# Kernel optimization log

Measured on AMD Instinct MI355X. Metric: run time of the kernel, lower is better.

The kernel has to match this reference:

```python
import jax, jax.numpy as jnp
import numpy as np

B, L, H = 32, 512, 1024
Q = 128
VA_H = 256

def setup_inputs() -> dict:
    key = jax.random.key(0)
    ks = jax.random.split(key, 12)
    hidden_states = jax.random.normal(ks[0], (B, L, H), dtype=jnp.float32)
    # Build valid inclusive spans: start in [2, L-16), length in [0, 8)
    asp_s = jax.random.randint(ks[1], (B, Q), 2, L - 16)
    asp_e = asp_s + jax.random.randint(ks[2], (B, Q), 0, 8)
    opi_s = jax.random.randint(ks[3], (B, Q), 2, L - 16)
    opi_e = opi_s + jax.random.randint(ks[4], (B, Q), 0, 8)
    null = jax.random.uniform(ks[5], (B, Q)) < 0.1
    asp_s = jnp.where(null, 0, asp_s)
    quad_spans = jnp.stack([asp_s, asp_e, opi_s, opi_e], axis=-1).astype(jnp.int64)
    quad_mask = (jax.random.uniform(ks[6], (B, Q)) > 0.3).astype(jnp.float32)
    # MLP params (torch Linear: y = x @ W.T + b), kaiming-ish scale
    def lin(k, out_d, in_d):
        return jax.random.normal(k, (out_d, in_d), dtype=jnp.float32) / np.sqrt(in_d)
    W1 = lin(ks[7], VA_H, 3 * H); b1 = jnp.zeros((VA_H,), jnp.float32)
    W2 = lin(ks[8], VA_H // 2, VA_H); b2 = jnp.zeros((VA_H // 2,), jnp.float32)
    W3 = lin(ks[9], 2, VA_H // 2); b3 = jnp.zeros((2,), jnp.float32)
    return {"hidden_states": hidden_states, "quad_spans": quad_spans,
            "quad_mask": quad_mask, "W1": W1, "b1": b1, "W2": W2, "b2": b2,
            "W3": W3, "b3": b3}

def _pool_spans(hidden_states, s, e):
    # hidden_states: [B,L,H]; s,e: [B,Q] inclusive indices
    pos = jnp.arange(hidden_states.shape[1])  # [L]
    valid = (s >= 2) & (e >= s)               # [B,Q]
    m = (pos[None, None, :] >= s[..., None]) & (pos[None, None, :] <= e[..., None])
    m = (m & valid[..., None]).astype(hidden_states.dtype)  # [B,Q,L]
    cnt = jnp.maximum(m.sum(-1, keepdims=True), 1.0)        # [B,Q,1]
    mean = jnp.einsum('bql,blh->bqh', m, hidden_states) / cnt
    sep = hidden_states[:, 1:2, :]                           # [B,1,H] fallback
    return jnp.where(valid[..., None], mean, sep)

def reference(hidden_states, quad_spans, quad_mask, W1, b1, W2, b2, W3, b3):
    h_asp = _pool_spans(hidden_states, quad_spans[..., 0], quad_spans[..., 1])
    h_opi = _pool_spans(hidden_states, quad_spans[..., 2], quad_spans[..., 3])
    h_pair = jnp.concatenate([h_asp, h_opi, h_asp * h_opi], axis=-1)  # [B,Q,3H]
    x = jax.nn.gelu(h_pair @ W1.T + b1, approximate=False)  # torch GELU = erf
    x = jax.nn.gelu(x @ W2.T + b2, approximate=False)
    va = jax.nn.sigmoid(x @ W3.T + b3) * 8.0 + 1.0          # [B,Q,2] in [1,9]
    # Invalid pairs stay zero, matching the torch loop's skipped entries
    return va * (quad_mask >= 0.5).astype(va.dtype)[..., None]
```

## Files before the change

kernel.cpp:

```cpp
#include <hip/hip_runtime.h>
#include <hip/hip_bf16.h>
#include <math.h>

typedef __bf16 bf16x8 __attribute__((ext_vector_type(8)));
typedef float f32x4 __attribute__((ext_vector_type(4)));

__device__ __forceinline__ unsigned short f2bf(float x) {
    union { float f; unsigned int u; } v; v.f = x;
    unsigned int r = v.u + 0x7fffu + ((v.u >> 16) & 1u);
    return (unsigned short)(r >> 16);
}
__device__ __forceinline__ float gelu_exact(float v) {
    return 0.5f * v * (1.0f + erff(v * 0.70710678118654752f));
}

__global__ __launch_bounds__(256) void prep_kernel(const float* __restrict__ hs,
                                                   const int* __restrict__ spans,
                                                   const float* __restrict__ W1,
                                                   const float* __restrict__ W2,
                                                   unsigned short* __restrict__ hp,
                                                   unsigned short* __restrict__ w1b,
                                                   unsigned short* __restrict__ w2b) {
    const int blk = blockIdx.x;
    const int tid = threadIdx.x;

    if (blk >= 4096) {
        if (blk < 4864) {
            const int i = (blk - 4096) * 256 + tid;
            float4 f = ((const float4*)W1)[i];
            ushort4 u;
            u.x = f2bf(f.x); u.y = f2bf(f.y); u.z = f2bf(f.z); u.w = f2bf(f.w);
            ((ushort4*)w1b)[i] = u;
        } else {
            const int i = (blk - 4864) * 256 + tid;
            float4 f = ((const float4*)W2)[i];
            ushort4 u;
            u.x = f2bf(f.x); u.y = f2bf(f.y); u.z = f2bf(f.z); u.w = f2bf(f.w);
            ((ushort4*)w2b)[i] = u;
        }
        return;
    }

    const int pair = blk;
    const int b = pair >> 7;

    const bool is64 = (spans[1] == 0);
    int s_a, e_a, s_o, e_o;
    if (is64) {
        s_a = spans[(pair * 4 + 0) * 2]; e_a = spans[(pair * 4 + 1) * 2];
        s_o = spans[(pair * 4 + 2) * 2]; e_o = spans[(pair * 4 + 3) * 2];
    } else {
        s_a = spans[pair * 4 + 0]; e_a = spans[pair * 4 + 1];
        s_o = spans[pair * 4 + 2]; e_o = spans[pair * 4 + 3];
    }

    if (!(s_a >= 2 && e_a >= s_a)) { s_a = 1; e_a = 1; }
    if (!(s_o >= 2 && e_o >= s_o)) { s_o = 1; e_o = 1; }
    const int lenA = e_a - s_a + 1;
    const int lenO = e_o - s_o + 1;

    const float4* base = (const float4*)hs + (size_t)b * 512 * 256;

    float4 va[8], vo[8];
#pragma unroll
    for (int t = 0; t < 8; ++t) {
        int ra = s_a + t; ra = (ra > e_a) ? e_a : ra;
        int ro = s_o + t; ro = (ro > e_o) ? e_o : ro;
        va[t] = base[ra * 256 + tid];
        vo[t] = base[ro * 256 + tid];
    }

    float4 A, O;
    {
        float ax = 0.f, ay = 0.f, az = 0.f, aw = 0.f;
        float ox = 0.f, oy = 0.f, oz = 0.f, ow = 0.f;
#pragma unroll
        for (int t = 0; t < 8; ++t) {
            const float wa = (t < lenA) ? 1.0f : 0.0f;
            const float wo = (t < lenO) ? 1.0f : 0.0f;
            ax += wa * va[t].x; ay += wa * va[t].y; az += wa * va[t].z; aw += wa * va[t].w;
            ox += wo * vo[t].x; oy += wo * vo[t].y; oz += wo * vo[t].z; ow += wo * vo[t].w;
        }
        const float ia = 1.0f / (float)lenA;
        const float io = 1.0f / (float)lenO;
        A.x = ax * ia; A.y = ay * ia; A.z = az * ia; A.w = aw * ia;
        O.x = ox * io; O.y = oy * io; O.z = oz * io; O.w = ow * io;
    }

    unsigned short* row = hp + (size_t)pair * 3072;
    const int d = tid * 4;
    ushort4 pa, po, pp;
    pa.x = f2bf(A.x); pa.y = f2bf(A.y); pa.z = f2bf(A.z); pa.w = f2bf(A.w);
    po.x = f2bf(O.x); po.y = f2bf(O.y); po.z = f2bf(O.z); po.w = f2bf(O.w);
    pp.x = f2bf(A.x * O.x); pp.y = f2bf(A.y * O.y);
    pp.z = f2bf(A.z * O.z); pp.w = f2bf(A.w * O.w);
    *(ushort4*)(row + d) = pa;
    *(ushort4*)(row + 1024 + d) = po;
    *(ushort4*)(row + 2048 + d) = pp;
}

__global__ __launch_bounds__(256, 2) void gemm1_gelu(const unsigned short* __restrict__ A,
                                                     const unsigned short* __restrict__ Bw,
                                                     const float* __restrict__ b1,
                                                     unsigned short* __restrict__ x1) {
    __shared__ __align__(16) unsigned short As[2 * 32 * 192];
    __shared__ __align__(16) unsigned short Bs[2 * 64 * 192];

    const int tid = threadIdx.x;
    const int lane = tid & 63;
    const int wid = tid >> 6;
    const int quad = lane >> 4;
    const int l16 = lane & 15;
    const int m0 = blockIdx.x * 32;
    const int n0 = blockIdx.y * 64;

    const unsigned short* Aptr[3];
#pragma unroll
    for (int p = 0; p < 3; ++p) {
        const int s = p * 256 + tid;
        const int row = s / 24;
        const int c = s - row * 24;
        const int lch = (c & 24) | ((c & 7) ^ (row & 7));
        Aptr[p] = A + (size_t)(m0 + row) * 3072 + lch * 8;
    }
    const unsigned short* Bptr[6];
#pragma unroll
    for (int p = 0; p < 6; ++p) {
        const int s = p * 256 + tid;
        const int row = s / 24;
        const int c = s - row * 24;
        const int lch = (c & 24) | ((c & 7) ^ (row & 7));
        Bptr[p] = Bw + (size_t)(n0 + row) * 3072 + lch * 8;
    }

    int aoff[2][6], boff[6];
#pragma unroll
    for (int h = 0; h < 6; ++h) {
        const int c = h * 4 + quad;
#pragma unroll
        for (int mh = 0; mh < 2; ++mh) {
            const int row = mh * 16 + l16;
            const int pc = (c & 24) | ((c & 7) ^ (row & 7));
            aoff[mh][h] = row * 192 + pc * 8;
        }
        const int brow = wid * 16 + l16;
        const int pcb = (c & 24) | ((c & 7) ^ (brow & 7));
        boff[h] = brow * 192 + pcb * 8;
    }

    f32x4 acc[2] = {};

#pragma unroll
    for (int p = 0; p < 3; ++p)
        __builtin_amdgcn_global_load_lds(
            (const __attribute__((address_space(1))) void*)Aptr[p],
            (__attribute__((address_space(3))) void*)(&As[(p * 256 + tid) * 8]), 16, 0, 0);
#pragma unroll
    for (int p = 0; p < 6; ++p)
        __builtin_amdgcn_global_load_lds(
            (const __attribute__((address_space(1))) void*)Bptr[p],
            (__attribute__((address_space(3))) void*)(&Bs[(p * 256 + tid) * 8]), 16, 0, 0);

    for (int it = 0; it < 16; ++it) {
        const int cur = it & 1;
        __syncthreads();
        if (it + 1 < 16) {
            const int nxt = cur ^ 1;
            const int kadv = (it + 1) * 192;
#pragma unroll
            for (int p = 0; p < 3; ++p)
                __builtin_amdgcn_global_load_lds(
                    (const __attribute__((address_space(1))) void*)(Aptr[p] + kadv),
                    (__attribute__((address_space(3))) void*)(&As[nxt * 6144 + (p * 256 + tid) * 8]), 16, 0, 0);
#pragma unroll
            for (int p = 0; p < 6; ++p)
                __builtin_amdgcn_global_load_lds(
                    (const __attribute__((address_space(1))) void*)(Bptr[p] + kadv),
                    (__attribute__((address_space(3))) void*)(&Bs[nxt * 12288 + (p * 256 + tid) * 8]), 16, 0, 0);
        }
#pragma unroll
        for (int h = 0; h < 6; ++h) {
            bf16x8 b = *(const bf16x8*)&Bs[cur * 12288 + boff[h]];
#pragma unroll
            for (int mh = 0; mh < 2; ++mh) {
                bf16x8 a = *(const bf16x8*)&As[cur * 6144 + aoff[mh][h]];
                acc[mh] = __builtin_amdgcn_mfma_f32_16x16x32_bf16(a, b, acc[mh], 0, 0, 0);
            }
        }
    }

    const int n = n0 + wid * 16 + l16;
    const float bn = b1[n];
#pragma unroll
    for (int mh = 0; mh < 2; ++mh) {
#pragma unroll
        for (int rr = 0; rr < 4; ++rr) {
            const int m = m0 + mh * 16 + quad * 4 + rr;
            x1[(size_t)m * 256 + n] = f2bf(gelu_exact(acc[mh][rr] + bn));
        }
    }
}

__global__ __launch_bounds__(256) void mlp2_head(const unsigned short* __restrict__ x1,
                                                 const unsigned short* __restrict__ w2b,
                                                 const float* __restrict__ b2,
                                                 const float* __restrict__ W3,
                                                 const float* __restrict__ b3,
                                                 const float* __restrict__ mask,
                                                 float* __restrict__ out) {
    __shared__ __align__(16) unsigned char smem[98304];
    unsigned short* Xs = (unsigned short*)smem;
    unsigned short* Ws = (unsigned short*)(smem + 16384);
    float*          X2 = (float*)(smem + 81920);

    const int tid = threadIdx.x;
    const int lane = tid & 63;
    const int wid = tid >> 6;
    const int quad = lane >> 4;
    const int l16 = lane & 15;
    const int wM = (wid >> 1) * 16;
    const int wN = (wid & 1) * 64;
    const int m0 = blockIdx.x * 32;

#pragma unroll
    for (int p = 0; p < 4; ++p) {
        const int s = p * 256 + tid;
        const int row = s >> 5;
        const int c = s & 31;
        const int lch = (c & 24) | ((c & 7) ^ (row & 7));
        __builtin_amdgcn_global_load_lds(
            (const __attribute__((address_space(1))) void*)(x1 + (size_t)(m0 + row) * 256 + lch * 8),
            (__attribute__((address_space(3))) void*)(&Xs[s * 8]), 16, 0, 0);
    }
#pragma unroll
    for (int p = 0; p < 16; ++p) {
        const int s = p * 256 + tid;
        const int row = s >> 5;
        const int c = s & 31;
        const int lch = (c & 24) | ((c & 7) ^ (row & 7));
        __builtin_amdgcn_global_load_lds(
            (const __attribute__((address_space(1))) void*)(w2b + (size_t)row * 256 + lch * 8),
            (__attribute__((address_space(3))) void*)(&Ws[s * 8]), 16, 0, 0);
    }
    __syncthreads();

    f32x4 acc[4] = {};
#pragma unroll
    for (int h = 0; h < 8; ++h) {
        const int c = h * 4 + quad;
        const int rowa = wM + l16;
        const int pca = (c & 24) | ((c & 7) ^ (rowa & 7));
        bf16x8 a = *(const bf16x8*)&Xs[rowa * 256 + pca * 8];
#pragma unroll
        for (int ni = 0; ni < 4; ++ni) {
            const int rowb = wN + ni * 16 + l16;
            const int pcb = (c & 24) | ((c & 7) ^ (rowb & 7));
            bf16x8 b = *(const bf16x8*)&Ws[rowb * 256 + pcb * 8];
            acc[ni] = __builtin_amdgcn_mfma_f32_16x16x32_bf16(a, b, acc[ni], 0, 0, 0);
        }
    }

#pragma unroll
    for (int ni = 0; ni < 4; ++ni) {
        const int n = wN + ni * 16 + l16;
        const float bn = b2[n];
#pragma unroll
        for (int rr = 0; rr < 4; ++rr) {
            const int m = wM + quad * 4 + rr;
            X2[m * 128 + n] = gelu_exact(acc[ni][rr] + bn);
        }
    }
    __syncthreads();

    const int p = tid >> 3;
    const int cc = (tid & 7) * 16;
    float a0 = 0.f, a1 = 0.f;
#pragma unroll
    for (int j = 0; j < 16; ++j) {
        const float xv = X2[p * 128 + cc + j];
        a0 += xv * W3[cc + j];
        a1 += xv * W3[128 + cc + j];
    }
    a0 += __shfl_xor(a0, 1); a0 += __shfl_xor(a0, 2); a0 += __shfl_xor(a0, 4);
    a1 += __shfl_xor(a1, 1); a1 += __shfl_xor(a1, 2); a1 += __shfl_xor(a1, 4);
    if ((tid & 7) == 0) {
        const int pair = m0 + p;
        const float mk = (mask[pair] >= 0.5f) ? 1.0f : 0.0f;
        out[pair * 2 + 0] = ((1.0f / (1.0f + expf(-(a0 + b3[0])))) * 8.0f + 1.0f) * mk;
        out[pair * 2 + 1] = ((1.0f / (1.0f + expf(-(a1 + b3[1])))) * 8.0f + 1.0f) * mk;
    }
}

extern "C" void kernel_launch(void* const* d_in, const int* in_sizes, int n_in,
                              void* d_out, int out_size, void* d_ws, size_t ws_size,
                              hipStream_t stream) {
    const float* hs   = (const float*)d_in[0];
    const int*   spans= (const int*)d_in[1];
    const float* mask = (const float*)d_in[2];
    const float* W1   = (const float*)d_in[3];
    const float* b1   = (const float*)d_in[4];
    const float* W2   = (const float*)d_in[5];
    const float* b2   = (const float*)d_in[6];
    const float* W3   = (const float*)d_in[7];
    const float* b3   = (const float*)d_in[8];
    float* out = (float*)d_out;

    unsigned short* hp  = (unsigned short*)d_ws;
    unsigned short* w1b = (unsigned short*)((char*)d_ws + 25165824);
    unsigned short* x1  = (unsigned short*)((char*)d_ws + 26738688);
    unsigned short* w2b = (unsigned short*)((char*)d_ws + 28835840);

    prep_kernel<<<dim3(4896), dim3(256), 0, stream>>>(hs, spans, W1, W2, hp, w1b, w2b);
    gemm1_gelu<<<dim3(128, 4), dim3(256), 0, stream>>>(hp, w1b, b1, x1);
    mlp2_head<<<dim3(128), dim3(256), 0, stream>>>(x1, w2b, b2, W3, b3, mask, out);
}
```

Before: 144.8 us.

## Fuse span pooling into GEMM1 with pipelined per-chunk pooling

Span mean pooling and pair construction now happen inside the first GEMM kernel. Pooled bf16 activations for 16 rows are produced chunk by chunk into shared memory, overlapped with double-buffered W1 staging. This removes the 24 MB intermediate hp buffer write and reread and one kernel launch. In exchange each block covers all 256 output columns for only 16 rows, so W1 is streamed by all 256 blocks, and only 128 of 512 threads do the pooling loads, which may limit gather bandwidth.

```diff
diff --git a/kernel.cpp b/kernel.cpp
--- a/kernel.cpp
+++ b/kernel.cpp
@@ -14,64 +14,80 @@
     return 0.5f * v * (1.0f + erff(v * 0.70710678118654752f));
 }
 
-__global__ __launch_bounds__(256) void prep_kernel(const float* __restrict__ hs,
-                                                   const int* __restrict__ spans,
-                                                   const float* __restrict__ W1,
-                                                   const float* __restrict__ W2,
-                                                   unsigned short* __restrict__ hp,
-                                                   unsigned short* __restrict__ w1b,
-                                                   unsigned short* __restrict__ w2b) {
+__global__ __launch_bounds__(256) void wconv(const float* __restrict__ W1,
+                                             const float* __restrict__ W2,
+                                             unsigned short* __restrict__ w1b,
+                                             unsigned short* __restrict__ w2b) {
     const int blk = blockIdx.x;
     const int tid = threadIdx.x;
-
-    if (blk >= 4096) {
-        if (blk < 4864) {
-            const int i = (blk - 4096) * 256 + tid;
-            float4 f = ((const float4*)W1)[i];
-            ushort4 u;
-            u.x = f2bf(f.x); u.y = f2bf(f.y); u.z = f2bf(f.z); u.w = f2bf(f.w);
-            ((ushort4*)w1b)[i] = u;
+    if (blk < 768) {
+        const int i = blk * 256 + tid;
+        float4 f = ((const float4*)W1)[i];
+        ushort4 u;
+        u.x = f2bf(f.x); u.y = f2bf(f.y); u.z = f2bf(f.z); u.w = f2bf(f.w);
+        ((ushort4*)w1b)[i] = u;
+    } else {
+        const int i = (blk - 768) * 256 + tid;
+        float4 f = ((const float4*)W2)[i];
+        ushort4 u;
+        u.x = f2bf(f.x); u.y = f2bf(f.y); u.z = f2bf(f.z); u.w = f2bf(f.w);
+        ((ushort4*)w2b)[i] = u;
+    }
+}
+
+__global__ __launch_bounds__(512, 2) void fused_pool_gemm1(
+        const float* __restrict__ hs,
+        const int* __restrict__ spans,
+        const unsigned short* __restrict__ w1b,
+        const float* __restrict__ b1,
+        unsigned short* __restrict__ x1) {
+    __shared__ __align__(16) unsigned short Bs[2][8192];
+    __shared__ __align__(16) unsigned short Ac[2][3][512];
+
+    const int tid = threadIdx.x;
+    const int lane = tid & 63;
+    const int wid = tid >> 6;
+    const int quad = lane >> 4;
+    const int l16 = lane & 15;
+    const int m0 = blockIdx.x * 16;
+
+    int sA = 1, eA = 1, sO = 1, eO = 1, lenA = 1, lenO = 1;
+    int f4 = 0, plocal = 0;
+    const float4* pbase = (const float4*)hs;
+    if (tid < 128) {
+        plocal = tid >> 3;
+        f4 = tid & 7;
+        const int pair = m0 + plocal;
+        const int b = pair >> 7;
+        const bool is64 = (spans[1] == 0);
+        int s_a, e_a, s_o, e_o;
+        if (is64) {
+            s_a = spans[(pair * 4 + 0) * 2]; e_a = spans[(pair * 4 + 1) * 2];
+            s_o = spans[(pair * 4 + 2) * 2]; e_o = spans[(pair * 4 + 3) * 2];
         } else {
-            const int i = (blk - 4864) * 256 + tid;
-            float4 f = ((const float4*)W2)[i];
-            ushort4 u;
-            u.x = f2bf(f.x); u.y = f2bf(f.y); u.z = f2bf(f.z); u.w = f2bf(f.w);
-            ((ushort4*)w2b)[i] = u;
-        }
-        return;
-    }
-
-    const int pair = blk;
-    const int b = pair >> 7;
-
-    const bool is64 = (spans[1] == 0);
-    int s_a, e_a, s_o, e_o;
-    if (is64) {
-        s_a = spans[(pair * 4 + 0) * 2]; e_a = spans[(pair * 4 + 1) * 2];
-        s_o = spans[(pair * 4 + 2) * 2]; e_o = spans[(pair * 4 + 3) * 2];
-    } else {
-        s_a = spans[pair * 4 + 0]; e_a = spans[pair * 4 + 1];
-        s_o = spans[pair * 4 + 2]; e_o = spans[pair * 4 + 3];
-    }
-
-    if (!(s_a >= 2 && e_a >= s_a)) { s_a = 1; e_a = 1; }
-    if (!(s_o >= 2 && e_o >= s_o)) { s_o = 1; e_o = 1; }
-    const int lenA = e_a - s_a + 1;
-    const int lenO = e_o - s_o + 1;
-
-    const float4* base = (const float4*)hs + (size_t)b * 512 * 256;
+            s_a = spans[pair * 4 + 0]; e_a = spans[pair * 4 + 1];
+            s_o = spans[pair * 4 + 2]; e_o = spans[pair * 4 + 3];
+        }
+        if (!(s_a >= 2 && e_a >= s_a)) { s_a = 1; e_a = 1; }
+        if (!(s_o >= 2 && e_o >= s_o)) { s_o = 1; e_o = 1; }
+        sA = s_a; eA = e_a; sO = s_o; eO = e_o;
+        lenA = eA - sA + 1; lenO = eO - sO + 1;
+        pbase = (const float4*)hs + (size_t)b * 512 * 256;
+    }
 
     float4 va[8], vo[8];
-#pragma unroll
-    for (int t = 0; t < 8; ++t) {
-        int ra = s_a + t; ra = (ra > e_a) ? e_a : ra;
-        int ro = s_o + t; ro = (ro > e_o) ? e_o : ro;
-        va[t] = base[ra * 256 + tid];
-        vo[t] = base[ro * 256 + tid];
-    }
-
-    float4 A, O;
-    {
+    auto POOL_LOAD = [&](int h) {
+        const int cb = h * 8 + f4;
+#pragma unroll
+        for (int t = 0; t < 8; ++t) {
+            int ra = sA + t; ra = (ra > eA) ? eA : ra;
+            int ro = sO + t; ro = (ro > eO) ? eO : ro;
+            va[t] = pbase[ra * 256 + cb];
+            vo[t] = pbase[ro * 256 + cb];
+        }
+    };
+    auto POOL_WRITE = [&](int h) {
+        const int buf = h & 1;
         float ax = 0.f, ay = 0.f, az = 0.f, aw = 0.f;
         float ox = 0.f, oy = 0.f, oz = 0.f, ow = 0.f;
 #pragma unroll
@@ -83,120 +99,70 @@
         }
         const float ia = 1.0f / (float)lenA;
         const float io = 1.0f / (float)lenO;
-        A.x = ax * ia; A.y = ay * ia; A.z = az * ia; A.w = aw * ia;
-        O.x = ox * io; O.y = oy * io; O.z = oz * io; O.w = ow * io;
-    }
-
-    unsigned short* row = hp + (size_t)pair * 3072;
-    const int d = tid * 4;
-    ushort4 pa, po, pp;
-    pa.x = f2bf(A.x); pa.y = f2bf(A.y); pa.z = f2bf(A.z); pa.w = f2bf(A.w);
-    po.x = f2bf(O.x); po.y = f2bf(O.y); po.z = f2bf(O.z); po.w = f2bf(O.w);
-    pp.x = f2bf(A.x * O.x); pp.y = f2bf(A.y * O.y);
-    pp.z = f2bf(A.z * O.z); pp.w = f2bf(A.w * O.w);
-    *(ushort4*)(row + d) = pa;
-    *(ushort4*)(row + 1024 + d) = po;
-    *(ushort4*)(row + 2048 + d) = pp;
-}
-
-__global__ __launch_bounds__(256, 2) void gemm1_gelu(const unsigned short* __restrict__ A,
-                                                     const unsigned short* __restrict__ Bw,
-                                                     const float* __restrict__ b1,
-                                                     unsigned short* __restrict__ x1) {
-    __shared__ __align__(16) unsigned short As[2 * 32 * 192];
-    __shared__ __align__(16) unsigned short Bs[2 * 64 * 192];
-
-    const int tid = threadIdx.x;
-    const int lane = tid & 63;
-    const int wid = tid >> 6;
-    const int quad = lane >> 4;
-    const int l16 = lane & 15;
-    const int m0 = blockIdx.x * 32;
-    const int n0 = blockIdx.y * 64;
-
-    const unsigned short* Aptr[3];
-#pragma unroll
-    for (int p = 0; p < 3; ++p) {
-        const int s = p * 256 + tid;
-        const int row = s / 24;
-        const int c = s - row * 24;
-        const int lch = (c & 24) | ((c & 7) ^ (row & 7));
-        Aptr[p] = A + (size_t)(m0 + row) * 3072 + lch * 8;
-    }
-    const unsigned short* Bptr[6];
-#pragma unroll
-    for (int p = 0; p < 6; ++p) {
-        const int s = p * 256 + tid;
-        const int row = s / 24;
-        const int c = s - row * 24;
-        const int lch = (c & 24) | ((c & 7) ^ (row & 7));
-        Bptr[p] = Bw + (size_t)(n0 + row) * 3072 + lch * 8;
-    }
-
-    int aoff[2][6], boff[6];
-#pragma unroll
-    for (int h = 0; h < 6; ++h) {
-        const int c = h * 4 + quad;
-#pragma unroll
-        for (int mh = 0; mh < 2; ++mh) {
-            const int row = mh * 16 + l16;
-            const int pc = (c & 24) | ((c & 7) ^ (row & 7));
-            aoff[mh][h] = row * 192 + pc * 8;
-        }
-        const int brow = wid * 16 + l16;
-        const int pcb = (c & 24) | ((c & 7) ^ (brow & 7));
-        boff[h] = brow * 192 + pcb * 8;
-    }
+        ax *= ia; ay *= ia; az *= ia; aw *= ia;
+        ox *= io; oy *= io; oz *= io; ow *= io;
+        ushort4 ua, uo, up;
+        ua.x = f2bf(ax); ua.y = f2bf(ay); ua.z = f2bf(az); ua.w = f2bf(aw);
+        uo.x = f2bf(ox); uo.y = f2bf(oy); uo.z = f2bf(oz); uo.w = f2bf(ow);
+        up.x = f2bf(ax * ox); up.y = f2bf(ay * oy);
+        up.z = f2bf(az * oz); up.w = f2bf(aw * ow);
+        const int off = plocal * 32 + f4 * 4;
+        *(ushort4*)&Ac[buf][0][off] = ua;
+        *(ushort4*)&Ac[buf][1][off] = uo;
+        *(ushort4*)&Ac[buf][2][off] = up;
+    };
+    auto B_STAGE = [&](int sec, int h, int buf) {
+        const int colbase = sec * 1024 + h * 32;
+#pragma unroll
+        for (int q = 0; q < 2; ++q) {
+            const int s = q * 512 + tid;
+            const int row = s >> 2;
+            const int c = s & 3;
+            __builtin_amdgcn_global_load_lds(
+                (const __attribute__((address_space(1))) void*)(w1b + (size_t)row * 3072 + colbase + c * 8),
+                (__attribute__((address_space(3))) void*)(&Bs[buf][s * 8]), 16, 0, 0);
+        }
+    };
 
     f32x4 acc[2] = {};
 
-#pragma unroll
-    for (int p = 0; p < 3; ++p)
-        __builtin_amdgcn_global_load_lds(
-            (const __attribute__((address_space(1))) void*)Aptr[p],
-            (__attribute__((address_space(3))) void*)(&As[(p * 256 + tid) * 8]), 16, 0, 0);
-#pragma unroll
-    for (int p = 0; p < 6; ++p)
-        __builtin_amdgcn_global_load_lds(
-            (const __attribute__((address_space(1))) void*)Bptr[p],
-            (__attribute__((address_space(3))) void*)(&Bs[(p * 256 + tid) * 8]), 16, 0, 0);
-
-    for (int it = 0; it < 16; ++it) {
-        const int cur = it & 1;
-        __syncthreads();
-        if (it + 1 < 16) {
-            const int nxt = cur ^ 1;
-            const int kadv = (it + 1) * 192;
-#pragma unroll
-            for (int p = 0; p < 3; ++p)
-                __builtin_amdgcn_global_load_lds(
-                    (const __attribute__((address_space(1))) void*)(Aptr[p] + kadv),
-                    (__attribute__((address_space(3))) void*)(&As[nxt * 6144 + (p * 256 + tid) * 8]), 16, 0, 0);
-#pragma unroll
-            for (int p = 0; p < 6; ++p)
-                __builtin_amdgcn_global_load_lds(
-                    (const __attribute__((address_space(1))) void*)(Bptr[p] + kadv),
-                    (__attribute__((address_space(3))) void*)(&Bs[nxt * 12288 + (p * 256 + tid) * 8]), 16, 0, 0);
-        }
-#pragma unroll
-        for (int h = 0; h < 6; ++h) {
-            bf16x8 b = *(const bf16x8*)&Bs[cur * 12288 + boff[h]];
-#pragma unroll
-            for (int mh = 0; mh < 2; ++mh) {
-                bf16x8 a = *(const bf16x8*)&As[cur * 6144 + aoff[mh][h]];
-                acc[mh] = __builtin_amdgcn_mfma_f32_16x16x32_bf16(a, b, acc[mh], 0, 0, 0);
+    if (tid < 128) POOL_LOAD(0);
+    B_STAGE(0, 0, 0);
+    __syncthreads();
+    if (tid < 128) { POOL_WRITE(0); POOL_LOAD(1); }
+
+    for (int h = 0; h < 32; ++h) {
+#pragma unroll
+        for (int sec = 0; sec < 3; ++sec) {
+            const int s = h * 3 + sec;
+            __syncthreads();
+            if (s + 1 < 96) {
+                const int nsec = (sec < 2) ? sec + 1 : 0;
+                const int nh = (sec < 2) ? h : h + 1;
+                B_STAGE(nsec, nh, (s + 1) & 1);
             }
-        }
-    }
-
-    const int n = n0 + wid * 16 + l16;
-    const float bn = b1[n];
-#pragma unroll
-    for (int mh = 0; mh < 2; ++mh) {
+            if (tid < 128) {
+                if (sec == 1 && h + 1 < 32) POOL_WRITE(h + 1);
+                if (sec == 2 && h + 2 < 32) POOL_LOAD(h + 2);
+            }
+            bf16x8 a = *(const bf16x8*)&Ac[h & 1][sec][l16 * 32 + quad * 8];
+#pragma unroll
+            for (int ni = 0; ni < 2; ++ni) {
+                const int brow = wid * 32 + ni * 16 + l16;
+                bf16x8 b = *(const bf16x8*)&Bs[s & 1][brow * 32 + quad * 8];
+                acc[ni] = __builtin_amdgcn_mfma_f32_16x16x32_bf16(a, b, acc[ni], 0, 0, 0);
+            }
+        }
+    }
+
+#pragma unroll
+    for (int ni = 0; ni < 2; ++ni) {
+        const int n = wid * 32 + ni * 16 + l16;
+        const float bn = b1[n];
 #pragma unroll
         for (int rr = 0; rr < 4; ++rr) {
-            const int m = m0 + mh * 16 + quad * 4 + rr;
-            x1[(size_t)m * 256 + n] = f2bf(gelu_exact(acc[mh][rr] + bn));
+            const int m = m0 + quad * 4 + rr;
+            x1[(size_t)m * 256 + n] = f2bf(gelu_exact(acc[ni][rr] + bn));
         }
     }
 }
@@ -305,12 +271,11 @@
     const float* b3   = (const float*)d_in[8];
     float* out = (float*)d_out;
 
-    unsigned short* hp  = (unsigned short*)d_ws;
     unsigned short* w1b = (unsigned short*)((char*)d_ws + 25165824);
     unsigned short* x1  = (unsigned short*)((char*)d_ws + 26738688);
     unsigned short* w2b = (unsigned short*)((char*)d_ws + 28835840);
 
-    prep_kernel<<<dim3(4896), dim3(256), 0, stream>>>(hs, spans, W1, W2, hp, w1b, w2b);
-    gemm1_gelu<<<dim3(128, 4), dim3(256), 0, stream>>>(hp, w1b, b1, x1);
+    wconv<<<dim3(800), dim3(256), 0, stream>>>(W1, W2, w1b, w2b);
+    fused_pool_gemm1<<<dim3(256), dim3(512), 0, stream>>>(hs, spans, w1b, b1, x1);
     mlp2_head<<<dim3(128), dim3(256), 0, stream>>>(x1, w2b, b2, W3, b3, mask, out);
 }
```

Result: slower. 163.1 us (+12.6%).
